# Performance work log

Hardware: AMD Instinct MI355X
Metric: run time of the kernel (lower is better)

Reference implementation:

```python
import jax, jax.numpy as jnp
import numpy as np

NUM_MODELS = 4
B = 16384
HIDDEN = 512
QDIM = 256
LAST_HIDDEN = 256
UW = 0.1          # uncertainty_weight
EPS = 1e-5        # LayerNorm eps (torch default)
FEAT_DIMS = [1024, 768, 512, 640]


def _linear(x, W, b):
    return x @ W.T + b


def _layernorm(h, g, b):
    mu = jnp.mean(h, axis=-1, keepdims=True)
    var = jnp.mean((h - mu) ** 2, axis=-1, keepdims=True)
    return (h - mu) * jax.lax.rsqrt(var + EPS) * g + b


def setup_inputs() -> dict:
    key = jax.random.key(0)
    ks = jax.random.split(key, 40)
    inp = {}
    for i, d in enumerate(FEAT_DIMS):
        inp[f"feat{i}"] = jax.random.normal(ks[i], (B, d), jnp.float32)
        inp[f"W_intra{i}"] = jax.random.normal(ks[4 + i], (HIDDEN, d), jnp.float32) / np.sqrt(d)
        inp[f"b_intra{i}"] = jnp.zeros((HIDDEN,), jnp.float32)
    inp["pred_scores"] = jax.random.uniform(ks[8], (B, NUM_MODELS), jnp.float32)
    inp["pred_vars"] = jax.random.uniform(ks[9], (B, NUM_MODELS), jnp.float32)
    inp["ln_g"] = jnp.ones((HIDDEN,), jnp.float32)
    inp["ln_b"] = jnp.zeros((HIDDEN,), jnp.float32)
    inp["Wq"] = jax.random.normal(ks[10], (QDIM, HIDDEN), jnp.float32) / np.sqrt(HIDDEN)
    inp["bq"] = jnp.zeros((QDIM,), jnp.float32)
    inp["Wk"] = jax.random.normal(ks[11], (QDIM, HIDDEN), jnp.float32) / np.sqrt(HIDDEN)
    inp["bk"] = jnp.zeros((QDIM,), jnp.float32)
    inp["Wv"] = jax.random.normal(ks[12], (QDIM, HIDDEN), jnp.float32) / np.sqrt(HIDDEN)
    inp["bv"] = jnp.zeros((QDIM,), jnp.float32)
    d1 = NUM_MODELS * QDIM + NUM_MODELS
    inp["W1"] = jax.random.normal(ks[13], (LAST_HIDDEN, d1), jnp.float32) / np.sqrt(d1)
    inp["b1"] = jnp.zeros((LAST_HIDDEN,), jnp.float32)
    inp["Wfc"] = jax.random.normal(ks[14], (1, LAST_HIDDEN), jnp.float32) / np.sqrt(LAST_HIDDEN)
    inp["bfc"] = jnp.zeros((1,), jnp.float32)
    return inp


def _forward(feats, pred_scores, pred_vars, W_intras, b_intras,
             ln_g, ln_b, Wq, bq, Wk, bk, Wv, bv, W1, b1, Wfc, bfc):
    # per-model branch: Linear -> ReLU -> (dropout=id) -> ReLU -> LayerNorm
    hiddens = []
    for i in range(NUM_MODELS):
        h = jax.nn.relu(_linear(feats[i], W_intras[i], b_intras[i]))
        h = jax.nn.relu(h)  # second relu after dropout (identity in eval)
        hiddens.append(_layernorm(h, ln_g, ln_b))
    H = jnp.stack(hiddens, axis=1)  # (B, M, HIDDEN)

    # cross-attention with uncertainty; NOTE source bug: key = drop(q) => keys == queries
    q = jnp.einsum('bmh,qh->bmq', H, Wq) + bq          # (B, M, Q)
    k = q                                              # faithful to `key = self.drop(q)`
    v = jnp.einsum('bmh,qh->bmq', H, Wv) + bv          # (B, M, Q)

    scores = jnp.einsum('biq,bjq->bij', q, k)          # (B, M, M)
    vars_ = pred_vars[:, None, :] + pred_vars[:, :, None]  # vars[b,i,j] = v[b,j] + v[b,i]
    scores = jax.nn.softmax(scores - UW * vars_, axis=-1)
    z = jnp.einsum('bij,bjq->biq', scores, v).reshape(B, NUM_MODELS * QDIM)

    out = jnp.concatenate([z, pred_scores], axis=-1)
    out = _linear(out, W1, b1)
    logits = _linear(out, Wfc, bfc)
    return jax.nn.sigmoid(logits)  # (B, 1)


def reference(feat0, feat1, feat2, feat3,
              W_intra0, b_intra0, W_intra1, b_intra1,
              W_intra2, b_intra2, W_intra3, b_intra3,
              pred_scores, pred_vars, ln_g, ln_b,
              Wq, bq, Wk, bk, Wv, bv, W1, b1, Wfc, bfc):
    feats = [feat0, feat1, feat2, feat3]
    W_intras = [W_intra0, W_intra1, W_intra2, W_intra3]
    b_intras = [b_intra0, b_intra1, b_intra2, b_intra3]
    return _forward(feats, pred_scores, pred_vars, W_intras, b_intras,
                    ln_g, ln_b, Wq, bq, Wk, bk, Wv, bv, W1, b1, Wfc, bfc)
```

## Files before the change

### kernel.cpp

```cpp
#include <hip/hip_runtime.h>
#include <hip/hip_bf16.h>


typedef __bf16 bf16;
typedef __bf16 bf16x4_t __attribute__((ext_vector_type(4)));
typedef __bf16 bf16x8_t __attribute__((ext_vector_type(8)));
typedef float  f32x4_t  __attribute__((ext_vector_type(4)));

__device__ __forceinline__ bf16x8_t cvt8(f32x4_t a, f32x4_t b) {
  bf16x8_t r;
  r[0] = (bf16)a[0]; r[1] = (bf16)a[1]; r[2] = (bf16)a[2]; r[3] = (bf16)a[3];
  r[4] = (bf16)b[0]; r[5] = (bf16)b[1]; r[6] = (bf16)b[2]; r[7] = (bf16)b[3];
  return r;
}

__device__ __forceinline__ void gl_lds16(const void* g, void* l) {
  __builtin_amdgcn_global_load_lds(
      (const __attribute__((address_space(1))) void*)g,
      (__attribute__((address_space(3))) void*)l, 16, 0, 0);
}

#define SBAR()   __builtin_amdgcn_s_barrier()
#define SCHED0() __builtin_amdgcn_sched_barrier(0)

__device__ __forceinline__ bf16x8_t frag_b16(const bf16* Ts, int row, int c0) {
  const int byte = row * 64 + ((c0 ^ ((row >> 1) & 3)) << 4);
  return *(const bf16x8_t*)((const char*)Ts + byte);
}
__device__ __forceinline__ void stage_b16(const bf16* __restrict__ src, int ld,
                                          int k0, bf16* lds) {
  const int l = threadIdx.x & 63;
  const int w = threadIdx.x >> 6;
#pragma unroll
  for (int j = 0; j < 2; ++j) {
    const int rb = w * 32 + j * 16;
    const int r  = rb + (l >> 2);
    const int sc = (l & 3) ^ ((r >> 1) & 3);
    gl_lds16(src + (size_t)r * ld + k0 + sc * 8, (char*)lds + rb * 64);
  }
}

__device__ __forceinline__ bf16x8_t frag_f32(const float* Ts, int row, int g) {
  const int p0 = (2 * g)     ^ (row & 7);
  const int p1 = (2 * g + 1) ^ (row & 7);
  f32x4_t lo = *(const f32x4_t*)((const char*)Ts + row * 128 + (p0 << 4));
  f32x4_t hi = *(const f32x4_t*)((const char*)Ts + row * 128 + (p1 << 4));
  return cvt8(lo, hi);
}
__device__ __forceinline__ void stage_f32(const float* __restrict__ src, int ld,
                                          int k0, float* lds) {
  const int l = threadIdx.x & 63;
  const int w = threadIdx.x >> 6;
#pragma unroll
  for (int j = 0; j < 4; ++j) {
    const int rb = w * 32 + j * 8;
    const int r  = rb + (l >> 3);
    const int q  = (l & 7) ^ (r & 7);
    gl_lds16(src + (size_t)r * ld + k0 + q * 4, (char*)lds + rb * 128);
  }
}

template<int AF32>
__device__ __forceinline__ void stage_deep(const void* A, int lda, const void* B,
                                           int ldb, int k0, char* buf) {
  if (AF32) {
    stage_f32((const float*)A, lda, k0, (float*)buf);
    stage_b16((const bf16*)B, ldb, k0, (bf16*)(buf + 16384));
  } else {
    stage_b16((const bf16*)A, lda, k0, (bf16*)buf);
    stage_f32((const float*)B, ldb, k0, (float*)(buf + 8192));
  }
}

template<int AF32>
__device__ __forceinline__ void mfma_deep(const char* buf, f32x4_t acc[4][4]) {
  const int lane = threadIdx.x & 63;
  const int wid  = threadIdx.x >> 6;
  const int wm = wid >> 1, wn = wid & 1;
  const int fr = lane & 15, g = lane >> 4;
  bf16x8_t ar[4], br[4];
  if (AF32) {
    const float* Af = (const float*)buf;
    const bf16*  Bb = (const bf16*)(buf + 16384);
#pragma unroll
    for (int mi = 0; mi < 4; ++mi) ar[mi] = frag_f32(Af, wm * 64 + mi * 16 + fr, g);
#pragma unroll
    for (int ni = 0; ni < 4; ++ni) br[ni] = frag_b16(Bb, wn * 64 + ni * 16 + fr, g);
  } else {
    const bf16*  Ab = (const bf16*)buf;
    const float* Bf = (const float*)(buf + 8192);
#pragma unroll
    for (int mi = 0; mi < 4; ++mi) ar[mi] = frag_b16(Ab, wm * 64 + mi * 16 + fr, g);
#pragma unroll
    for (int ni = 0; ni < 4; ++ni) br[ni] = frag_f32(Bf, wn * 64 + ni * 16 + fr, g);
  }
#pragma unroll
  for (int mi = 0; mi < 4; ++mi)
#pragma unroll
    for (int ni = 0; ni < 4; ++ni)
      acc[mi][ni] = __builtin_amdgcn_mfma_f32_16x16x32_bf16(ar[mi], br[ni], acc[mi][ni], 0, 0, 0);
}

template<int AF32>
__device__ __forceinline__ void core_deep3(const void* A, int lda, const void* B,
                                           int ldb, int K, char* lds,
                                           f32x4_t acc[4][4]) {
  const int nt = K >> 5;
  stage_deep<AF32>(A, lda, B, ldb, 0,  lds);
  stage_deep<AF32>(A, lda, B, ldb, 32, lds + 24576);
  stage_deep<AF32>(A, lda, B, ldb, 64, lds + 49152);
  int buf = 0;
  for (int t = 0; t < nt; ++t) {
    const int ahead = nt - 1 - t;
    if (ahead >= 2)      asm volatile("s_waitcnt vmcnt(12)" ::: "memory");
    else if (ahead == 1) asm volatile("s_waitcnt vmcnt(6)"  ::: "memory");
    else                 asm volatile("s_waitcnt vmcnt(0)"  ::: "memory");
    SBAR(); SCHED0();
    __builtin_amdgcn_s_setprio(1);
    mfma_deep<AF32>(lds + buf * 24576, acc);
    __builtin_amdgcn_s_setprio(0);
    SCHED0(); SBAR();
    if (t + 3 < nt) stage_deep<AF32>(A, lda, B, ldb, (t + 3) * 32, lds + buf * 24576);
    buf = (buf == 2) ? 0 : buf + 1;
  }
}

template<int RELU>
__device__ __forceinline__ void epi_bf16(f32x4_t acc[4][4], bf16* __restrict__ C, int ldc,
                                         const float* __restrict__ bias) {
  const int lane = threadIdx.x & 63;
  const int wid  = threadIdx.x >> 6;
  const int wm = wid >> 1, wn = wid & 1;
  const int fr = lane & 15;
  const int rb = wm * 64 + 4 * (lane >> 4);
  const int cb = wn * 64 + fr;
  float bv[4];
#pragma unroll
  for (int ni = 0; ni < 4; ++ni) bv[ni] = bias[cb + ni * 16];
#pragma unroll
  for (int mi = 0; mi < 4; ++mi)
#pragma unroll
    for (int j = 0; j < 4; ++j)
#pragma unroll
      for (int ni = 0; ni < 4; ++ni) {
        float val = acc[mi][ni][j] + bv[ni];
        if (RELU) val = fmaxf(val, 0.f);
        C[(size_t)(rb + mi * 16 + j) * ldc + cb + ni * 16] = (bf16)val;
      }
}

__device__ __forceinline__ void cp8(bf16* d, const float* s) {
  f32x4_t x0 = *(const f32x4_t*)s;
  f32x4_t x1 = *(const f32x4_t*)(s + 4);
  *(bf16x8_t*)d = cvt8(x0, x1);
}

__global__ __launch_bounds__(256) void prep_kernel(
    const float* __restrict__ w0, const float* __restrict__ w1s,
    const float* __restrict__ w2, const float* __restrict__ w3,
    bf16* __restrict__ o0, bf16* __restrict__ o1,
    bf16* __restrict__ o2, bf16* __restrict__ o3) {
  const int t = blockIdx.x * 256 + threadIdx.x;
  if (t < 65536)       { size_t i = (size_t)t * 8;            cp8(o0 + i, w0 + i); }
  else if (t < 114688) { size_t i = (size_t)(t - 65536) * 8;  cp8(o1 + i, w1s + i); }
  else if (t < 147456) { size_t i = (size_t)(t - 114688) * 8; cp8(o2 + i, w2 + i); }
  else                 { size_t i = (size_t)(t - 147456) * 8; cp8(o3 + i, w3 + i); }
}

__global__ __launch_bounds__(256) void intra_kernel(
    const float* __restrict__ f0, const float* __restrict__ f1,
    const float* __restrict__ f2, const float* __restrict__ f3,
    const bf16* __restrict__ wb0, const bf16* __restrict__ wb1,
    const bf16* __restrict__ wb2, const bf16* __restrict__ wb3,
    const float* __restrict__ bb0, const float* __restrict__ bb1,
    const float* __restrict__ bb2, const float* __restrict__ bb3,
    bf16* __restrict__ hbuf) {
  __shared__ __align__(16) char lds[73728];
  const int bid = blockIdx.x;
  const int lid = (bid & 7) * 256 + (bid >> 3);
  const int x = lid & 3;
  const int g = lid >> 2;
  const int z = g & 3;
  const int y = g >> 2;
  const float* fp; const bf16* wp; const float* bp; int K;
  switch (z) {
    case 0:  fp = f0; wp = wb0; bp = bb0; K = 1024; break;
    case 1:  fp = f1; wp = wb1; bp = bb1; K = 768;  break;
    case 2:  fp = f2; wp = wb2; bp = bb2; K = 512;  break;
    default: fp = f3; wp = wb3; bp = bb3; K = 640;  break;
  }
  f32x4_t acc[4][4];
#pragma unroll
  for (int i = 0; i < 4; ++i)
#pragma unroll
    for (int j = 0; j < 4; ++j) acc[i][j] = (f32x4_t){0.f, 0.f, 0.f, 0.f};
  core_deep3<1>(fp + (size_t)(y * 128) * K, K,
                wp + (size_t)(x * 128) * K, K, K, lds, acc);
  bf16* C = hbuf + (size_t)(y * 128) * 2048 + z * 512 + x * 128;
  epi_bf16<1>(acc, C, 2048, bp + x * 128);
}

__global__ __launch_bounds__(256)
void ln_kernel(bf16* __restrict__ h, const float* __restrict__ g,
               const float* __restrict__ bta) {
  const int row  = blockIdx.x * 4 + (threadIdx.x >> 6);
  const int lane = threadIdx.x & 63;
  bf16* p = h + (size_t)row * 512 + lane * 8;
  const bf16x8_t x = *(const bf16x8_t*)p;
  float xf[8]; float s = 0.f, s2 = 0.f;
#pragma unroll
  for (int j = 0; j < 8; ++j) { xf[j] = (float)x[j]; s += xf[j]; s2 += xf[j] * xf[j]; }
#pragma unroll
  for (int off = 1; off < 64; off <<= 1) { s += __shfl_xor(s, off); s2 += __shfl_xor(s2, off); }
  const float mu  = s * (1.f / 512.f);
  const float var = s2 * (1.f / 512.f) - mu * mu;
  const float inv = rsqrtf(var + 1e-5f);
  f32x4_t g0 = *(const f32x4_t*)(g + lane * 8);
  f32x4_t g1 = *(const f32x4_t*)(g + lane * 8 + 4);
  f32x4_t b0 = *(const f32x4_t*)(bta + lane * 8);
  f32x4_t b1 = *(const f32x4_t*)(bta + lane * 8 + 4);
  bf16x8_t o;
#pragma unroll
  for (int j = 0; j < 4; ++j) o[j]     = (bf16)((xf[j] - mu) * inv * g0[j] + b0[j]);
#pragma unroll
  for (int j = 0; j < 4; ++j) o[4 + j] = (bf16)((xf[4 + j] - mu) * inv * g1[j] + b1[j]);
  *(bf16x8_t*)p = o;
}

__global__ __launch_bounds__(256) void qv_kernel(
    const bf16* __restrict__ H, const float* __restrict__ Wq,
    const float* __restrict__ Wv, const float* __restrict__ bq,
    const float* __restrict__ bv, bf16* __restrict__ qvout) {
  __shared__ __align__(16) char lds[73728];
  const int bid = blockIdx.x;
  const int lid = (bid & 7) * 256 + (bid >> 3);
  const int x = lid & 3, y = lid >> 2;
  const float* Wsrc = (x < 2) ? Wq : Wv;
  f32x4_t acc[4][4];
#pragma unroll
  for (int i = 0; i < 4; ++i)
#pragma unroll
    for (int j = 0; j < 4; ++j) acc[i][j] = (f32x4_t){0.f, 0.f, 0.f, 0.f};
  core_deep3<0>(H + (size_t)(y * 128) * 512, 512,
                Wsrc + (size_t)((x & 1) * 128) * 512, 512, 512, lds, acc);
  const float* bias = (x < 2) ? bq + x * 128 : bv + (x - 2) * 128;
  epi_bf16<0>(acc, qvout + (size_t)(y * 128) * 512 + x * 128, 512, bias);
}

__global__ __launch_bounds__(256) void w1_kernel(
    const bf16* __restrict__ zb, const float* __restrict__ W1,
    const float* __restrict__ b1, const float* __restrict__ ps,
    float* __restrict__ obuf) {
  __shared__ __align__(16) char lds[73728];
  const int bid = blockIdx.x;
  const int lid = (bid & 7) * 32 + (bid >> 3);
  const int x = lid & 1, y = lid >> 1;
  f32x4_t acc[4][4];
#pragma unroll
  for (int i = 0; i < 4; ++i)
#pragma unroll
    for (int j = 0; j < 4; ++j) acc[i][j] = (f32x4_t){0.f, 0.f, 0.f, 0.f};
  core_deep3<0>(zb + (size_t)(y * 128) * 1024, 1024,
                W1 + (size_t)(x * 128) * 1028, 1028, 1024, lds, acc);

  const int lane = threadIdx.x & 63;
  const int wid  = threadIdx.x >> 6;
  const int wm = wid >> 1, wn = wid & 1;
  const int fr = lane & 15;
  const int rb = wm * 64 + 4 * (lane >> 4);
  const int cb = x * 128 + wn * 64 + fr;
  float bv[4], wt[4][4];
#pragma unroll
  for (int ni = 0; ni < 4; ++ni) {
    bv[ni] = b1[cb + ni * 16];
#pragma unroll
    for (int m = 0; m < 4; ++m) wt[ni][m] = W1[(size_t)(cb + ni * 16) * 1028 + 1024 + m];
  }
#pragma unroll
  for (int mi = 0; mi < 4; ++mi)
#pragma unroll
    for (int j = 0; j < 4; ++j) {
      const int r = y * 128 + rb + mi * 16 + j;
      f32x4_t psv = *(const f32x4_t*)(ps + (size_t)r * 4);
#pragma unroll
      for (int ni = 0; ni < 4; ++ni) {
        float val = acc[mi][ni][j] + bv[ni]
                  + psv[0] * wt[ni][0] + psv[1] * wt[ni][1]
                  + psv[2] * wt[ni][2] + psv[3] * wt[ni][3];
        obuf[(size_t)r * 256 + cb + ni * 16] = val;
      }
    }
}

__global__ __launch_bounds__(256)
void attn_kernel(const bf16* __restrict__ qv, const float* __restrict__ pvars,
                 bf16* __restrict__ z) {
  const int b    = blockIdx.x * 4 + (threadIdx.x >> 6);
  const int lane = threadIdx.x & 63;
  float qf[4][4], vf[4][4];
#pragma unroll
  for (int i = 0; i < 4; ++i) {
    const bf16* row = qv + ((size_t)b * 4 + i) * 512;
    bf16x4_t qq = *(const bf16x4_t*)(row + lane * 4);
    bf16x4_t vv = *(const bf16x4_t*)(row + 256 + lane * 4);
#pragma unroll
    for (int c = 0; c < 4; ++c) { qf[i][c] = (float)qq[c]; vf[i][c] = (float)vv[c]; }
  }
  float s[4][4];
#pragma unroll
  for (int i = 0; i < 4; ++i)
#pragma unroll
    for (int j = 0; j < 4; ++j)
      s[i][j] = qf[i][0] * qf[j][0] + qf[i][1] * qf[j][1] + qf[i][2] * qf[j][2] + qf[i][3] * qf[j][3];
#pragma unroll
  for (int off = 1; off < 64; off <<= 1)
#pragma unroll
    for (int i = 0; i < 4; ++i)
#pragma unroll
      for (int j = 0; j < 4; ++j) s[i][j] += __shfl_xor(s[i][j], off);

  float var4[4];
#pragma unroll
  for (int m = 0; m < 4; ++m) var4[m] = pvars[(size_t)b * 4 + m];
  float w[4][4];
#pragma unroll
  for (int i = 0; i < 4; ++i) {
    float t[4]; float mx = -1e30f;
#pragma unroll
    for (int j = 0; j < 4; ++j) { t[j] = s[i][j] - 0.1f * (var4[i] + var4[j]); mx = fmaxf(mx, t[j]); }
    float sum = 0.f;
#pragma unroll
    for (int j = 0; j < 4; ++j) { t[j] = expf(t[j] - mx); sum += t[j]; }
    const float is = 1.f / sum;
#pragma unroll
    for (int j = 0; j < 4; ++j) w[i][j] = t[j] * is;
  }
#pragma unroll
  for (int i = 0; i < 4; ++i) {
    bf16x4_t zo;
#pragma unroll
    for (int c = 0; c < 4; ++c) {
      float zf = w[i][0] * vf[0][c] + w[i][1] * vf[1][c] + w[i][2] * vf[2][c] + w[i][3] * vf[3][c];
      zo[c] = (bf16)zf;
    }
    *(bf16x4_t*)(z + ((size_t)b * 4 + i) * 256 + lane * 4) = zo;
  }
}

__global__ __launch_bounds__(256)
void fc_kernel(const float* __restrict__ o, const float* __restrict__ wfc,
               const float* __restrict__ bfc, float* __restrict__ out) {
  const int b    = blockIdx.x * 4 + (threadIdx.x >> 6);
  const int lane = threadIdx.x & 63;
  f32x4_t ov = *(const f32x4_t*)(o + (size_t)b * 256 + lane * 4);
  f32x4_t wv = *(const f32x4_t*)(wfc + lane * 4);
  float p = ov[0] * wv[0] + ov[1] * wv[1] + ov[2] * wv[2] + ov[3] * wv[3];
#pragma unroll
  for (int off = 1; off < 64; off <<= 1) p += __shfl_xor(p, off);
  if (lane == 0) {
    const float lg = p + bfc[0];
    out[b] = 1.f / (1.f + expf(-lg));
  }
}

extern "C" void kernel_launch(void* const* d_in, const int* in_sizes, int n_in,
                              void* d_out, int out_size, void* d_ws, size_t ws_size,
                              hipStream_t stream) {
  (void)in_sizes; (void)n_in; (void)out_size; (void)ws_size;
  const float* feat[4] = {(const float*)d_in[0], (const float*)d_in[3],
                          (const float*)d_in[6], (const float*)d_in[9]};
  const float* Wi[4]   = {(const float*)d_in[1], (const float*)d_in[4],
                          (const float*)d_in[7], (const float*)d_in[10]};
  const float* bi[4]   = {(const float*)d_in[2], (const float*)d_in[5],
                          (const float*)d_in[8], (const float*)d_in[11]};
  const float* ps  = (const float*)d_in[12];
  const float* pv  = (const float*)d_in[13];
  const float* lng = (const float*)d_in[14];
  const float* lnb = (const float*)d_in[15];
  const float* Wq  = (const float*)d_in[16];
  const float* bq  = (const float*)d_in[17];
  const float* Wv  = (const float*)d_in[20];
  const float* bvp = (const float*)d_in[21];
  const float* W1  = (const float*)d_in[22];
  const float* b1  = (const float*)d_in[23];
  const float* Wfc = (const float*)d_in[24];
  const float* bfc = (const float*)d_in[25];

  char* ws = (char*)d_ws;
  const size_t MB = 1024 * 1024;
  bf16*  hbuf  = (bf16*)ws;
  bf16*  zbuf  = (bf16*)ws;
  float* obuf  = (float*)(ws + 32 * MB);
  bf16*  wb0   = (bf16*)(ws + 64 * MB);
  bf16*  wb1   = (bf16*)(ws + 65 * MB);
  bf16*  wb2   = (bf16*)(ws + 65 * MB + 786432);
  bf16*  wb3   = (bf16*)(ws + 66 * MB + 262144);
  bf16*  qvout = (bf16*)(ws + 64 * MB);

  hipLaunchKernelGGL(prep_kernel, dim3(736), dim3(256), 0, stream,
                     Wi[0], Wi[1], Wi[2], Wi[3], wb0, wb1, wb2, wb3);
  hipLaunchKernelGGL(intra_kernel, dim3(2048), dim3(256), 0, stream,
                     feat[0], feat[1], feat[2], feat[3],
                     wb0, wb1, wb2, wb3, bi[0], bi[1], bi[2], bi[3], hbuf);
  hipLaunchKernelGGL(ln_kernel, dim3(65536 / 4), dim3(256), 0, stream, hbuf, lng, lnb);
  hipLaunchKernelGGL(qv_kernel, dim3(2048), dim3(256), 0, stream,
                     hbuf, Wq, Wv, bq, bvp, qvout);
  hipLaunchKernelGGL(attn_kernel, dim3(16384 / 4), dim3(256), 0, stream, qvout, pv, zbuf);
  hipLaunchKernelGGL(w1_kernel, dim3(256), dim3(256), 0, stream, zbuf, W1, b1, ps, obuf);
  hipLaunchKernelGGL(fc_kernel, dim3(16384 / 4), dim3(256), 0, stream, obuf, Wfc, bfc, (float*)d_out);
}
```

Before: 256.4 us.

## Widen intra GEMM tiles to 128x512 so each fp32 feature row is read once

The intra-branch GEMM now uses 512-thread blocks that each compute a full 128x512 output tile, covering all hidden columns, instead of four 128x128 tiles. Each fp32 feature tile is therefore loaded from global memory once rather than four times, cutting the dominant fp32 activation traffic. The K loop becomes a two-stage double-buffered global-to-LDS pipeline, replacing the previous deeper one. Only 512 blocks are launched with larger per-wave accumulators (8x4), so occupancy and latency hiding may suffer.

```diff
diff --git a/kernel.cpp b/kernel.cpp
--- a/kernel.cpp
+++ b/kernel.cpp
@@ -27,25 +27,25 @@
   const int byte = row * 64 + ((c0 ^ ((row >> 1) & 3)) << 4);
   return *(const bf16x8_t*)((const char*)Ts + byte);
 }
-__device__ __forceinline__ void stage_b16(const bf16* __restrict__ src, int ld,
-                                          int k0, bf16* lds) {
-  const int l = threadIdx.x & 63;
-  const int w = threadIdx.x >> 6;
-#pragma unroll
-  for (int j = 0; j < 2; ++j) {
-    const int rb = w * 32 + j * 16;
-    const int r  = rb + (l >> 2);
-    const int sc = (l & 3) ^ ((r >> 1) & 3);
-    gl_lds16(src + (size_t)r * ld + k0 + sc * 8, (char*)lds + rb * 64);
-  }
-}
-
 __device__ __forceinline__ bf16x8_t frag_f32(const float* Ts, int row, int g) {
   const int p0 = (2 * g)     ^ (row & 7);
   const int p1 = (2 * g + 1) ^ (row & 7);
   f32x4_t lo = *(const f32x4_t*)((const char*)Ts + row * 128 + (p0 << 4));
   f32x4_t hi = *(const f32x4_t*)((const char*)Ts + row * 128 + (p1 << 4));
   return cvt8(lo, hi);
+}
+
+__device__ __forceinline__ void stage_b16(const bf16* __restrict__ src, int ld,
+                                          int k0, bf16* lds) {
+  const int l = threadIdx.x & 63;
+  const int w = threadIdx.x >> 6;
+#pragma unroll
+  for (int j = 0; j < 2; ++j) {
+    const int rb = w * 32 + j * 16;
+    const int r  = rb + (l >> 2);
+    const int sc = (l & 3) ^ ((r >> 1) & 3);
+    gl_lds16(src + (size_t)r * ld + k0 + sc * 8, (char*)lds + rb * 64);
+  }
 }
 __device__ __forceinline__ void stage_f32(const float* __restrict__ src, int ld,
                                           int k0, float* lds) {
@@ -149,6 +149,121 @@
       }
 }
 
+__device__ __forceinline__ void stage_f32_512(const float* __restrict__ src, int ld,
+                                              int k0, float* lds) {
+  const int l = threadIdx.x & 63;
+  const int w = threadIdx.x >> 6;
+#pragma unroll
+  for (int j = 0; j < 2; ++j) {
+    const int rb = w * 16 + j * 8;
+    const int r  = rb + (l >> 3);
+    const int q  = (l & 7) ^ (r & 7);
+    gl_lds16(src + (size_t)r * ld + k0 + q * 4, (char*)lds + rb * 128);
+  }
+}
+__device__ __forceinline__ void stage_b16_512(const bf16* __restrict__ src, int ld,
+                                              int k0, bf16* lds) {
+  const int l = threadIdx.x & 63;
+  const int w = threadIdx.x >> 6;
+#pragma unroll
+  for (int j = 0; j < 4; ++j) {
+    const int rb = w * 64 + j * 16;
+    const int r  = rb + (l >> 2);
+    const int sc = (l & 3) ^ ((r >> 1) & 3);
+    gl_lds16(src + (size_t)r * ld + k0 + sc * 8, (char*)lds + rb * 64);
+  }
+}
+
+__device__ __forceinline__ void mfma_512(const char* buf, f32x4_t acc[8][4]) {
+  const int lane = threadIdx.x & 63;
+  const int wn   = threadIdx.x >> 6;
+  const int fr = lane & 15, g = lane >> 4;
+  const float* Af = (const float*)buf;
+  const bf16*  Bb = (const bf16*)(buf + 16384);
+  bf16x8_t ar[8], br[4];
+#pragma unroll
+  for (int mi = 0; mi < 8; ++mi) ar[mi] = frag_f32(Af, mi * 16 + fr, g);
+#pragma unroll
+  for (int ni = 0; ni < 4; ++ni) br[ni] = frag_b16(Bb, wn * 64 + ni * 16 + fr, g);
+#pragma unroll
+  for (int mi = 0; mi < 8; ++mi)
+#pragma unroll
+    for (int ni = 0; ni < 4; ++ni)
+      acc[mi][ni] = __builtin_amdgcn_mfma_f32_16x16x32_bf16(ar[mi], br[ni], acc[mi][ni], 0, 0, 0);
+}
+
+__global__ __launch_bounds__(512, 2) void intra_kernel(
+    const float* __restrict__ f0, const float* __restrict__ f1,
+    const float* __restrict__ f2, const float* __restrict__ f3,
+    const bf16* __restrict__ wb0, const bf16* __restrict__ wb1,
+    const bf16* __restrict__ wb2, const bf16* __restrict__ wb3,
+    const float* __restrict__ bb0, const float* __restrict__ bb1,
+    const float* __restrict__ bb2, const float* __restrict__ bb3,
+    bf16* __restrict__ hbuf) {
+  __shared__ __align__(16) char lds[98304];
+  const int bid = blockIdx.x;
+  const int lid = (bid & 7) * 64 + (bid >> 3);
+  const int z = lid & 3;
+  const int y = lid >> 2;
+  const float* fp; const bf16* wp; const float* bp; int K;
+  switch (z) {
+    case 0:  fp = f0; wp = wb0; bp = bb0; K = 1024; break;
+    case 1:  fp = f1; wp = wb1; bp = bb1; K = 768;  break;
+    case 2:  fp = f2; wp = wb2; bp = bb2; K = 512;  break;
+    default: fp = f3; wp = wb3; bp = bb3; K = 640;  break;
+  }
+  const float* A = fp + (size_t)(y * 128) * K;
+  const bf16*  B = wp;
+
+  f32x4_t acc[8][4];
+#pragma unroll
+  for (int i = 0; i < 8; ++i)
+#pragma unroll
+    for (int j = 0; j < 4; ++j) acc[i][j] = (f32x4_t){0.f, 0.f, 0.f, 0.f};
+
+  const int nt = K >> 5;
+  char* buf0 = lds;
+  char* buf1 = lds + 49152;
+  stage_f32_512(A, K, 0, (float*)buf0);
+  stage_b16_512(B, K, 0, (bf16*)(buf0 + 16384));
+  stage_f32_512(A, K, 32, (float*)buf1);
+  stage_b16_512(B, K, 32, (bf16*)(buf1 + 16384));
+  for (int t = 0; t < nt; ++t) {
+    char* cur = (t & 1) ? buf1 : buf0;
+    if (t + 1 < nt) asm volatile("s_waitcnt vmcnt(6)" ::: "memory");
+    else            asm volatile("s_waitcnt vmcnt(0)" ::: "memory");
+    SBAR(); SCHED0();
+    __builtin_amdgcn_s_setprio(1);
+    mfma_512(cur, acc);
+    __builtin_amdgcn_s_setprio(0);
+    SCHED0(); SBAR();
+    if (t + 2 < nt) {
+      stage_f32_512(A, K, (t + 2) * 32, (float*)cur);
+      stage_b16_512(B, K, (t + 2) * 32, (bf16*)(cur + 16384));
+    }
+  }
+
+  const int lane = threadIdx.x & 63;
+  const int wn   = threadIdx.x >> 6;
+  const int fr = lane & 15;
+  const int rb = 4 * (lane >> 4);
+  float bv[4];
+#pragma unroll
+  for (int ni = 0; ni < 4; ++ni) bv[ni] = bp[wn * 64 + ni * 16 + fr];
+  bf16* C = hbuf + (size_t)(y * 128) * 2048 + z * 512;
+#pragma unroll
+  for (int mi = 0; mi < 8; ++mi)
+#pragma unroll
+    for (int j = 0; j < 4; ++j) {
+      const int row = mi * 16 + rb + j;
+#pragma unroll
+      for (int ni = 0; ni < 4; ++ni) {
+        float val = fmaxf(acc[mi][ni][j] + bv[ni], 0.f);
+        C[(size_t)row * 2048 + wn * 64 + ni * 16 + fr] = (bf16)val;
+      }
+    }
+}
+
 __device__ __forceinline__ void cp8(bf16* d, const float* s) {
   f32x4_t x0 = *(const f32x4_t*)s;
   f32x4_t x1 = *(const f32x4_t*)(s + 4);
@@ -165,39 +280,6 @@
   else if (t < 114688) { size_t i = (size_t)(t - 65536) * 8;  cp8(o1 + i, w1s + i); }
   else if (t < 147456) { size_t i = (size_t)(t - 114688) * 8; cp8(o2 + i, w2 + i); }
   else                 { size_t i = (size_t)(t - 147456) * 8; cp8(o3 + i, w3 + i); }
-}
-
-__global__ __launch_bounds__(256) void intra_kernel(
-    const float* __restrict__ f0, const float* __restrict__ f1,
-    const float* __restrict__ f2, const float* __restrict__ f3,
-    const bf16* __restrict__ wb0, const bf16* __restrict__ wb1,
-    const bf16* __restrict__ wb2, const bf16* __restrict__ wb3,
-    const float* __restrict__ bb0, const float* __restrict__ bb1,
-    const float* __restrict__ bb2, const float* __restrict__ bb3,
-    bf16* __restrict__ hbuf) {
-  __shared__ __align__(16) char lds[73728];
-  const int bid = blockIdx.x;
-  const int lid = (bid & 7) * 256 + (bid >> 3);
-  const int x = lid & 3;
-  const int g = lid >> 2;
-  const int z = g & 3;
-  const int y = g >> 2;
-  const float* fp; const bf16* wp; const float* bp; int K;
-  switch (z) {
-    case 0:  fp = f0; wp = wb0; bp = bb0; K = 1024; break;
-    case 1:  fp = f1; wp = wb1; bp = bb1; K = 768;  break;
-    case 2:  fp = f2; wp = wb2; bp = bb2; K = 512;  break;
-    default: fp = f3; wp = wb3; bp = bb3; K = 640;  break;
-  }
-  f32x4_t acc[4][4];
-#pragma unroll
-  for (int i = 0; i < 4; ++i)
-#pragma unroll
-    for (int j = 0; j < 4; ++j) acc[i][j] = (f32x4_t){0.f, 0.f, 0.f, 0.f};
-  core_deep3<1>(fp + (size_t)(y * 128) * K, K,
-                wp + (size_t)(x * 128) * K, K, K, lds, acc);
-  bf16* C = hbuf + (size_t)(y * 128) * 2048 + z * 512 + x * 128;
-  epi_bf16<1>(acc, C, 2048, bp + x * 128);
 }
 
 __global__ __launch_bounds__(256)
@@ -399,7 +481,7 @@
 
   hipLaunchKernelGGL(prep_kernel, dim3(736), dim3(256), 0, stream,
                      Wi[0], Wi[1], Wi[2], Wi[3], wb0, wb1, wb2, wb3);
-  hipLaunchKernelGGL(intra_kernel, dim3(2048), dim3(256), 0, stream,
+  hipLaunchKernelGGL(intra_kernel, dim3(512), dim3(512), 0, stream,
                      feat[0], feat[1], feat[2], feat[3],
                      wb0, wb1, wb2, wb3, bi[0], bi[1], bi[2], bi[3], hbuf);
   hipLaunchKernelGGL(ln_kernel, dim3(65536 / 4), dim3(256), 0, stream, hbuf, lng, lnb);
```

After: 252.6 us. No clear change (-1.5%).
